# Kernel optimization log

Measured on AMD Instinct MI355X. Metric: run time of the kernel, lower is better.

The kernel has to match this reference:

```python
import jax, jax.numpy as jnp
import numpy as np

ATOM_TYPES = (1, 6, 7, 8)  # H, C, N, O
BN_EPS = 1e-3


def setup_inputs() -> dict:
    key = jax.random.key(0)
    k1, k2, k3 = jax.random.split(key, 3)
    B, N, M, d, L = 16, 2048, 64, 3, 12
    X = jax.random.normal(k1, (B, N, d), jnp.float32) * 4.0  # coords in Angstrom-ish scale
    # neighbor indices; offset trick guarantees no self-neighbor (avoids R=0)
    off = jax.random.randint(k2, (B, N, M), 1, N)
    Nbrs = ((jnp.arange(N)[None, :, None] + off) % N).astype(jnp.int32)
    Nbrs_Z = jax.random.randint(k3, (B, N, M), 0, 10).astype(jnp.int32)
    params = np.array([[rc, rs, 4.0] for rc in (4.0, 8.0) for rs in (0.0, 1.0, 2.0, 3.0, 4.0, 5.0)], np.float32)
    rc = jnp.asarray(params[:, 0].reshape(L, 1, 1, 1))
    rs = jnp.asarray(params[:, 1].reshape(L, 1, 1, 1))
    re = jnp.asarray(params[:, 2].reshape(L, 1, 1, 1))
    return {"X": X, "Nbrs": Nbrs, "Nbrs_Z": Nbrs_Z, "rc": rc, "rs": rs, "re": re}


def reference(X, Nbrs, Nbrs_Z, rc, rs, re):
    # gather neighbor coordinates: [B,N,M,d]
    nbr = jax.vmap(lambda coords, idx: coords[idx])(X, Nbrs)
    D = nbr - X[:, :, None, :]                      # displacement tensor [B,N,M,d]
    R = jnp.sqrt(jnp.sum(D * D, axis=-1))           # distance matrix  [B,N,M]
    R1 = R[None]                                    # [1,B,N,M], broadcasts vs [L,1,1,1]
    K = jnp.exp(-re * (R1 - rs) ** 2)               # gaussian        [L,B,N,M]
    FC = jnp.where(R1 <= rc, 0.5 * (jnp.cos(jnp.pi * R1 / rc) + 1.0), 0.0)
    rsf = K * FC                                    # radial symmetry fn [L,B,N,M]
    # per-atom-type masks [A,B,N,M]
    types = jnp.asarray(ATOM_TYPES, Nbrs_Z.dtype)
    conds = (Nbrs_Z[None] == types[:, None, None, None]).astype(rsf.dtype)
    # masked reduce over neighbors, concat over types (type-major) -> [A*L,B,N]
    sym = jnp.einsum('abnm,lbnm->albn', conds, rsf)
    A, L = sym.shape[0], sym.shape[1]
    layer = sym.reshape(A * L, sym.shape[2], sym.shape[3]).transpose(1, 2, 0)  # [B,N,A*L]
    # tf.nn.moments over axis 0 (biased variance) + batch_normalization (no scale/offset)
    m = jnp.mean(layer, axis=0)
    v = jnp.var(layer, axis=0)
    return (layer - m) / jnp.sqrt(v + BN_EPS)
```

## Files before the change

kernel.cpp:

```cpp
#include <hip/hip_runtime.h>

#define NB 16
#define NN 2048
#define NM 64
#define NC 48
#define LDSP 49
#define PIF 3.14159265358979323f

struct F3 { float x, y, z; };

__device__ __forceinline__ void rc_pass(
    const float R[4], const int zs[4],
    float rcX, float pioX, float rc8, int grp,
    float nre, float gcoef, float rs3,
    float qu4, float qu5, float qd2, float qd1, float qd0,
    int b, int t, float* __restrict__ sBN)
{
  float2 acc2[12];
#pragma unroll
  for (int q = 0; q < 12; ++q) acc2[q] = make_float2(0.f, 0.f);

#pragma unroll
  for (int u = 0; u < 4; ++u) {
    const float Rv = R[u];
    const float Rk = fminf(Rv, rc8);

    const float u3 = Rk - rs3;
    const float K3 = __expf(nre * (u3 * u3));
    const float Gu = __expf(gcoef * Rk);
    const float Gd = __builtin_amdgcn_rcpf(Gu);
    const float K4 = K3 * Gu * qu4;
    const float K5 = K4 * Gu * qu5;
    const float K2 = K3 * Gd * qd2;
    const float K1 = K2 * Gd * qd1;
    const float K0 = K1 * Gd * qd0;
    const float K[6] = {K0, K1, K2, K3, K4, K5};

    const float cX  = __cosf(pioX * Rv);
    const float fcX = (Rv <= rcX) ? fmaf(0.5f, cX, 0.5f) : 0.f;

    const int z = zs[u];
    const float a0 = (z == 1) ? fcX : 0.f;
    const float a1 = (z == 6) ? fcX : 0.f;
    const float a2 = (z == 7) ? fcX : 0.f;
    const float a3 = (z == 8) ? fcX : 0.f;

#pragma unroll
    for (int p = 0; p < 3; ++p) {
      const float k0 = K[2 * p], k1 = K[2 * p + 1];
      acc2[0 + p].x = fmaf(a0, k0, acc2[0 + p].x);
      acc2[0 + p].y = fmaf(a0, k1, acc2[0 + p].y);
      acc2[3 + p].x = fmaf(a1, k0, acc2[3 + p].x);
      acc2[3 + p].y = fmaf(a1, k1, acc2[3 + p].y);
      acc2[6 + p].x = fmaf(a2, k0, acc2[6 + p].x);
      acc2[6 + p].y = fmaf(a2, k1, acc2[6 + p].y);
      acc2[9 + p].x = fmaf(a3, k0, acc2[9 + p].x);
      acc2[9 + p].y = fmaf(a3, k1, acc2[9 + p].y);
    }
  }

  float acc[24];
#pragma unroll
  for (int q = 0; q < 12; ++q) {
    acc[2 * q]     = acc2[q].x;
    acc[2 * q + 1] = acc2[q].y;
  }

#pragma unroll
  for (int c = 0; c < 24; ++c) acc[c] += __shfl_xor(acc[c], 8, 64);
  const bool s8 = (t & 8) != 0;
#pragma unroll
  for (int j = 0; j < 12; ++j) acc[j] = s8 ? acc[12 + j] : acc[j];
#pragma unroll
  for (int j = 0; j < 12; ++j) acc[j] += __shfl_xor(acc[j], 4, 64);
  const bool s4 = (t & 4) != 0;
#pragma unroll
  for (int j = 0; j < 6; ++j) acc[j] = s4 ? acc[6 + j] : acc[j];
#pragma unroll
  for (int j = 0; j < 6; ++j) acc[j] += __shfl_xor(acc[j], 2, 64);
  const bool s2 = (t & 2) != 0;
#pragma unroll
  for (int j = 0; j < 3; ++j) acc[j] = s2 ? acc[3 + j] : acc[j];
#pragma unroll
  for (int j = 0; j < 3; ++j) acc[j] += __shfl_xor(acc[j], 1, 64);

  const int ty = 2 * ((t >> 3) & 1) + ((t >> 2) & 1);
  const int r0 = 3 * ((t >> 1) & 1);
  const int gb = b * LDSP + ty * 12 + grp * 6 + r0;
  if (t & 1) {
    sBN[gb + 2] = acc[2];
  } else {
    sBN[gb + 0] = acc[0];
    sBN[gb + 1] = acc[1];
  }
}

__global__ __launch_bounds__(256, 8) void fused_kernel(
    const float* __restrict__ X,
    const int* __restrict__ Nbrs,
    const int* __restrict__ NbrsZ,
    const float* __restrict__ rcg,
    const float* __restrict__ rsg,
    const float* __restrict__ reg,
    float* __restrict__ out)
{
  __shared__ float sBN[NB * LDSP];

  const int tid = threadIdx.x;
  const int b   = tid >> 4;
  const int t   = tid & 15;
  const int n   = blockIdx.x;
  const int row = b * NN + n;

  const int base = row * NM + t * 4;
  const int4 j4 = *(const int4*)(Nbrs  + base);
  const int4 z4 = *(const int4*)(NbrsZ + base);

  const float rc4 = rcg[0], rc8 = rcg[6];
  const float re  = reg[0];
  const float nre = -re;
  const float pio4  = PIF / rc4;
  const float pio8  = PIF / rc8;
  const float sp    = rsg[1] - rsg[0];
  const float gcoef = 2.f * re * sp;
  const float rs3   = rsg[3];
  const float qu4 = __expf(nre * (rsg[4] * rsg[4] - rsg[3] * rsg[3]));
  const float qu5 = __expf(nre * (rsg[5] * rsg[5] - rsg[4] * rsg[4]));
  const float qd2 = __expf(nre * (rsg[2] * rsg[2] - rsg[3] * rsg[3]));
  const float qd1 = __expf(nre * (rsg[1] * rsg[1] - rsg[2] * rsg[2]));
  const float qd0 = __expf(nre * (rsg[0] * rsg[0] - rsg[1] * rsg[1]));

  const float* xb = X + (size_t)b * (NN * 3);
  const float xi = xb[n * 3 + 0];
  const float yi = xb[n * 3 + 1];
  const float zi = xb[n * 3 + 2];

  const int js[4] = {j4.x, j4.y, j4.z, j4.w};
  const int zs[4] = {z4.x, z4.y, z4.z, z4.w};

  float R[4];
#pragma unroll
  for (int u = 0; u < 4; ++u) {
    const F3 p = *(const F3*)(xb + js[u] * 3);
    const float dx = p.x - xi, dy = p.y - yi, dz = p.z - zi;
    R[u] = sqrtf(fmaf(dx, dx, fmaf(dy, dy, dz * dz)));
  }

  rc_pass(R, zs, rc4, pio4, rc8, 0, nre, gcoef, rs3,
          qu4, qu5, qd2, qd1, qd0, b, t, sBN);
  rc_pass(R, zs, rc8, pio8, rc8, 1, nre, gcoef, rs3,
          qu4, qu5, qd2, qd1, qd0, b, t, sBN);

  __syncthreads();

  if (tid < NC) {
    const int cc = tid;
    float x[NB];
    float s = 0.f;
#pragma unroll
    for (int bb = 0; bb < NB; ++bb) {
      x[bb] = sBN[bb * LDSP + cc];
      s += x[bb];
    }
    const float mean = s * (1.f / NB);
    float vs = 0.f;
#pragma unroll
    for (int bb = 0; bb < NB; ++bb) {
      const float d = x[bb] - mean;
      vs = fmaf(d, d, vs);
    }
    const float inv = rsqrtf(vs * (1.f / NB) + 1e-3f);
#pragma unroll
    for (int bb = 0; bb < NB; ++bb) {
      out[(size_t)bb * (NN * NC) + n * NC + cc] = (x[bb] - mean) * inv;
    }
  }
}

extern "C" void kernel_launch(void* const* d_in, const int* in_sizes, int n_in,
                              void* d_out, int out_size, void* d_ws, size_t ws_size,
                              hipStream_t stream) {
  const float* X   = (const float*)d_in[0];
  const int* Nbrs  = (const int*)d_in[1];
  const int* NbrsZ = (const int*)d_in[2];
  const float* rcg = (const float*)d_in[3];
  const float* rsg = (const float*)d_in[4];
  const float* reg = (const float*)d_in[5];

  float* out = (float*)d_out;

  fused_kernel<<<2048, 256, 0, stream>>>(X, Nbrs, NbrsZ, rcg, rsg, reg, out);
}
```

Before: 22.22 us.

## Split cutoff groups across half-rows and derive the rc4 cosine from rc8

```diff
diff --git a/kernel.cpp b/kernel.cpp
--- a/kernel.cpp
+++ b/kernel.cpp
@@ -9,90 +9,8 @@
 
 struct F3 { float x, y, z; };
 
-__device__ __forceinline__ void rc_pass(
-    const float R[4], const int zs[4],
-    float rcX, float pioX, float rc8, int grp,
-    float nre, float gcoef, float rs3,
-    float qu4, float qu5, float qd2, float qd1, float qd0,
-    int b, int t, float* __restrict__ sBN)
-{
-  float2 acc2[12];
-#pragma unroll
-  for (int q = 0; q < 12; ++q) acc2[q] = make_float2(0.f, 0.f);
-
-#pragma unroll
-  for (int u = 0; u < 4; ++u) {
-    const float Rv = R[u];
-    const float Rk = fminf(Rv, rc8);
-
-    const float u3 = Rk - rs3;
-    const float K3 = __expf(nre * (u3 * u3));
-    const float Gu = __expf(gcoef * Rk);
-    const float Gd = __builtin_amdgcn_rcpf(Gu);
-    const float K4 = K3 * Gu * qu4;
-    const float K5 = K4 * Gu * qu5;
-    const float K2 = K3 * Gd * qd2;
-    const float K1 = K2 * Gd * qd1;
-    const float K0 = K1 * Gd * qd0;
-    const float K[6] = {K0, K1, K2, K3, K4, K5};
-
-    const float cX  = __cosf(pioX * Rv);
-    const float fcX = (Rv <= rcX) ? fmaf(0.5f, cX, 0.5f) : 0.f;
-
-    const int z = zs[u];
-    const float a0 = (z == 1) ? fcX : 0.f;
-    const float a1 = (z == 6) ? fcX : 0.f;
-    const float a2 = (z == 7) ? fcX : 0.f;
-    const float a3 = (z == 8) ? fcX : 0.f;
-
-#pragma unroll
-    for (int p = 0; p < 3; ++p) {
-      const float k0 = K[2 * p], k1 = K[2 * p + 1];
-      acc2[0 + p].x = fmaf(a0, k0, acc2[0 + p].x);
-      acc2[0 + p].y = fmaf(a0, k1, acc2[0 + p].y);
-      acc2[3 + p].x = fmaf(a1, k0, acc2[3 + p].x);
-      acc2[3 + p].y = fmaf(a1, k1, acc2[3 + p].y);
-      acc2[6 + p].x = fmaf(a2, k0, acc2[6 + p].x);
-      acc2[6 + p].y = fmaf(a2, k1, acc2[6 + p].y);
-      acc2[9 + p].x = fmaf(a3, k0, acc2[9 + p].x);
-      acc2[9 + p].y = fmaf(a3, k1, acc2[9 + p].y);
-    }
-  }
-
-  float acc[24];
-#pragma unroll
-  for (int q = 0; q < 12; ++q) {
-    acc[2 * q]     = acc2[q].x;
-    acc[2 * q + 1] = acc2[q].y;
-  }
-
-#pragma unroll
-  for (int c = 0; c < 24; ++c) acc[c] += __shfl_xor(acc[c], 8, 64);
-  const bool s8 = (t & 8) != 0;
-#pragma unroll
-  for (int j = 0; j < 12; ++j) acc[j] = s8 ? acc[12 + j] : acc[j];
-#pragma unroll
-  for (int j = 0; j < 12; ++j) acc[j] += __shfl_xor(acc[j], 4, 64);
-  const bool s4 = (t & 4) != 0;
-#pragma unroll
-  for (int j = 0; j < 6; ++j) acc[j] = s4 ? acc[6 + j] : acc[j];
-#pragma unroll
-  for (int j = 0; j < 6; ++j) acc[j] += __shfl_xor(acc[j], 2, 64);
-  const bool s2 = (t & 2) != 0;
-#pragma unroll
-  for (int j = 0; j < 3; ++j) acc[j] = s2 ? acc[3 + j] : acc[j];
-#pragma unroll
-  for (int j = 0; j < 3; ++j) acc[j] += __shfl_xor(acc[j], 1, 64);
-
-  const int ty = 2 * ((t >> 3) & 1) + ((t >> 2) & 1);
-  const int r0 = 3 * ((t >> 1) & 1);
-  const int gb = b * LDSP + ty * 12 + grp * 6 + r0;
-  if (t & 1) {
-    sBN[gb + 2] = acc[2];
-  } else {
-    sBN[gb + 0] = acc[0];
-    sBN[gb + 1] = acc[1];
-  }
+__device__ __forceinline__ float rfl(float v) {
+  return __uint_as_float(__builtin_amdgcn_readfirstlane(__float_as_uint(v)));
 }
 
 __global__ __launch_bounds__(256, 8) void fused_kernel(
@@ -109,60 +27,132 @@
   const int tid = threadIdx.x;
   const int b   = tid >> 4;
   const int t   = tid & 15;
+  const int s   = t & 7;
+  const int h   = t >> 3;
   const int n   = blockIdx.x;
   const int row = b * NN + n;
-
-  const int base = row * NM + t * 4;
-  const int4 j4 = *(const int4*)(Nbrs  + base);
-  const int4 z4 = *(const int4*)(NbrsZ + base);
 
   const float rc4 = rcg[0], rc8 = rcg[6];
   const float re  = reg[0];
   const float nre = -re;
-  const float pio4  = PIF / rc4;
-  const float pio8  = PIF / rc8;
+  const float pio8  = rfl(PIF / rc8);
   const float sp    = rsg[1] - rsg[0];
-  const float gcoef = 2.f * re * sp;
+  const float gcoef = rfl(2.f * re * sp);
   const float rs3   = rsg[3];
-  const float qu4 = __expf(nre * (rsg[4] * rsg[4] - rsg[3] * rsg[3]));
-  const float qu5 = __expf(nre * (rsg[5] * rsg[5] - rsg[4] * rsg[4]));
-  const float qd2 = __expf(nre * (rsg[2] * rsg[2] - rsg[3] * rsg[3]));
-  const float qd1 = __expf(nre * (rsg[1] * rsg[1] - rsg[2] * rsg[2]));
-  const float qd0 = __expf(nre * (rsg[0] * rsg[0] - rsg[1] * rsg[1]));
+  const float qu4 = rfl(__expf(nre * (rsg[4] * rsg[4] - rsg[3] * rsg[3])));
+  const float qu5 = rfl(__expf(nre * (rsg[5] * rsg[5] - rsg[4] * rsg[4])));
+  const float qd2 = rfl(__expf(nre * (rsg[2] * rsg[2] - rsg[3] * rsg[3])));
+  const float qd1 = rfl(__expf(nre * (rsg[1] * rsg[1] - rsg[2] * rsg[2])));
+  const float qd0 = rfl(__expf(nre * (rsg[0] * rsg[0] - rsg[1] * rsg[1])));
 
   const float* xb = X + (size_t)b * (NN * 3);
   const float xi = xb[n * 3 + 0];
   const float yi = xb[n * 3 + 1];
   const float zi = xb[n * 3 + 2];
 
-  const int js[4] = {j4.x, j4.y, j4.z, j4.w};
-  const int zs[4] = {z4.x, z4.y, z4.z, z4.w};
+  float2 acc2[12];
+#pragma unroll
+  for (int q = 0; q < 12; ++q) acc2[q] = make_float2(0.f, 0.f);
 
-  float R[4];
 #pragma unroll
-  for (int u = 0; u < 4; ++u) {
-    const F3 p = *(const F3*)(xb + js[u] * 3);
-    const float dx = p.x - xi, dy = p.y - yi, dz = p.z - zi;
-    R[u] = sqrtf(fmaf(dx, dx, fmaf(dy, dy, dz * dz)));
+  for (int chunk = 0; chunk < 2; ++chunk) {
+    const int base = row * NM + s * 8 + chunk * 4;
+    const int4 j4 = *(const int4*)(Nbrs  + base);
+    const int4 z4 = *(const int4*)(NbrsZ + base);
+    const int js[4] = {j4.x, j4.y, j4.z, j4.w};
+    const int zs[4] = {z4.x, z4.y, z4.z, z4.w};
+
+    float R[4];
+#pragma unroll
+    for (int u = 0; u < 4; ++u) {
+      const F3 p = *(const F3*)(xb + js[u] * 3);
+      const float dx = p.x - xi, dy = p.y - yi, dz = p.z - zi;
+      R[u] = sqrtf(fmaf(dx, dx, fmaf(dy, dy, dz * dz)));
+    }
+
+#pragma unroll
+    for (int u = 0; u < 4; ++u) {
+      const float Rv = R[u];
+      const float Rk = fminf(Rv, rc8);
+
+      const float u3 = Rk - rs3;
+      const float K3 = __expf(nre * (u3 * u3));
+      const float Gu = __expf(gcoef * Rk);
+      const float Gd = __builtin_amdgcn_rcpf(Gu);
+      const float K4 = K3 * Gu * qu4;
+      const float K5 = K4 * Gu * qu5;
+      const float K2 = K3 * Gd * qd2;
+      const float K1 = K2 * Gd * qd1;
+      const float K0 = K1 * Gd * qd0;
+      const float K[6] = {K0, K1, K2, K3, K4, K5};
+
+      const float c8  = __cosf(pio8 * Rv);
+      const float c4  = fmaf(c8 + c8, c8, -1.f);
+      const float fc8 = (Rv <= rc8) ? fmaf(0.5f, c8, 0.5f) : 0.f;
+      const float fc4 = (Rv <= rc4) ? fmaf(0.5f, c4, 0.5f) : 0.f;
+      const float fcX = h ? fc8 : fc4;
+
+      const int z = zs[u];
+      const float a0 = (z == 1) ? fcX : 0.f;
+      const float a1 = (z == 6) ? fcX : 0.f;
+      const float a2 = (z == 7) ? fcX : 0.f;
+      const float a3 = (z == 8) ? fcX : 0.f;
+
+#pragma unroll
+      for (int p = 0; p < 3; ++p) {
+        const float k0 = K[2 * p], k1 = K[2 * p + 1];
+        acc2[0 + p].x = fmaf(a0, k0, acc2[0 + p].x);
+        acc2[0 + p].y = fmaf(a0, k1, acc2[0 + p].y);
+        acc2[3 + p].x = fmaf(a1, k0, acc2[3 + p].x);
+        acc2[3 + p].y = fmaf(a1, k1, acc2[3 + p].y);
+        acc2[6 + p].x = fmaf(a2, k0, acc2[6 + p].x);
+        acc2[6 + p].y = fmaf(a2, k1, acc2[6 + p].y);
+        acc2[9 + p].x = fmaf(a3, k0, acc2[9 + p].x);
+        acc2[9 + p].y = fmaf(a3, k1, acc2[9 + p].y);
+      }
+    }
   }
 
-  rc_pass(R, zs, rc4, pio4, rc8, 0, nre, gcoef, rs3,
-          qu4, qu5, qd2, qd1, qd0, b, t, sBN);
-  rc_pass(R, zs, rc8, pio8, rc8, 1, nre, gcoef, rs3,
-          qu4, qu5, qd2, qd1, qd0, b, t, sBN);
+  float acc[24];
+#pragma unroll
+  for (int q = 0; q < 12; ++q) {
+    acc[2 * q]     = acc2[q].x;
+    acc[2 * q + 1] = acc2[q].y;
+  }
+
+#pragma unroll
+  for (int c = 0; c < 24; ++c) acc[c] += __shfl_xor(acc[c], 4, 64);
+  const bool s4 = (s & 4) != 0;
+#pragma unroll
+  for (int j = 0; j < 12; ++j) acc[j] = s4 ? acc[12 + j] : acc[j];
+#pragma unroll
+  for (int j = 0; j < 12; ++j) acc[j] += __shfl_xor(acc[j], 2, 64);
+  const bool s2 = (s & 2) != 0;
+#pragma unroll
+  for (int j = 0; j < 6; ++j) acc[j] = s2 ? acc[6 + j] : acc[j];
+#pragma unroll
+  for (int j = 0; j < 6; ++j) acc[j] += __shfl_xor(acc[j], 1, 64);
+  const bool s1 = (s & 1) != 0;
+#pragma unroll
+  for (int j = 0; j < 3; ++j) acc[j] = s1 ? acc[3 + j] : acc[j];
+
+  const int gb = b * LDSP + (s >> 1) * 12 + h * 6 + 3 * (s & 1);
+  sBN[gb + 0] = acc[0];
+  sBN[gb + 1] = acc[1];
+  sBN[gb + 2] = acc[2];
 
   __syncthreads();
 
   if (tid < NC) {
     const int cc = tid;
     float x[NB];
-    float s = 0.f;
+    float sm = 0.f;
 #pragma unroll
     for (int bb = 0; bb < NB; ++bb) {
       x[bb] = sBN[bb * LDSP + cc];
-      s += x[bb];
+      sm += x[bb];
     }
-    const float mean = s * (1.f / NB);
+    const float mean = sm * (1.f / NB);
     float vs = 0.f;
 #pragma unroll
     for (int bb = 0; bb < NB; ++bb) {
```

After: 20.86 us. 1.07x faster.
